# Performance work log

Measured on AMD Instinct MI355X. Metric: run time of the kernel, lower is better.

The kernel has to match this reference:

```python
import jax, jax.numpy as jnp
import numpy as np

B, S, E = 2, 1024, 1024
H, DH = 16, 64           # num_heads, key_dim = E // H
MAXLEN = 2048            # config.max_sequence_length -> table size 2*MAXLEN-1


def setup_inputs() -> dict:
    key = jax.random.key(0)
    ks = jax.random.split(key, 13)
    sc = 1.0 / np.sqrt(E)
    return {
        "query": jax.random.normal(ks[0], (B, S, E), jnp.float32),
        "key": jax.random.normal(ks[1], (B, S, E), jnp.float32),
        "value": jax.random.normal(ks[2], (B, S, E), jnp.float32),
        "Wq": jax.random.normal(ks[3], (E, E), jnp.float32) * sc,
        "bq": jnp.zeros((E,), jnp.float32),
        "Wk": jax.random.normal(ks[4], (E, E), jnp.float32) * sc,
        "bk": jnp.zeros((E,), jnp.float32),
        "Wv": jax.random.normal(ks[5], (E, E), jnp.float32) * sc,
        "bv": jnp.zeros((E,), jnp.float32),
        "Wo": jax.random.normal(ks[6], (E, E), jnp.float32) * sc,
        "bo": jnp.zeros((E,), jnp.float32),
        "rel_pos_emb": jax.random.normal(ks[7], (2 * MAXLEN - 1, DH), jnp.float32) * 0.02,
        "rel_pos_bias": jnp.zeros((2 * MAXLEN - 1,), jnp.float32),
    }


def _split_heads(x):
    # [B, S, E] -> [B, H, S, DH]
    return x.reshape(B, S, H, DH).transpose(0, 2, 1, 3)


def _relative_shift(x):
    # x: [B, H, S, S]; pad one zero column on the left of the last dim,
    # reshape to [B, H, S+1, S], drop the first row -> [B, H, S, S]
    x = jnp.pad(x, ((0, 0), (0, 0), (0, 0), (1, 0)))
    x = x.reshape(B, H, S + 1, S)
    return x[:, :, 1:, :]


def reference(query, key, value, Wq, bq, Wk, bk, Wv, bv, Wo, bo,
              rel_pos_emb, rel_pos_bias):
    q = _split_heads(query @ Wq + bq) / jnp.sqrt(jnp.float32(DH))  # [B,H,S,DH]
    k = _split_heads(key @ Wk + bk)                                 # [B,H,S,DH]
    v = _split_heads(value @ Wv + bv)                               # [B,H,S,DH]

    scores = jnp.einsum("bhid,bhjd->bhij", q, k)  # [B,H,S,S]

    # relative position term (gather + skew, as in the original call())
    pos_ids = jnp.arange(S)[:, None] - jnp.arange(S)[None, :] + (MAXLEN - 1)  # [S,S]
    rpe = rel_pos_emb[pos_ids]    # [S, S, DH]
    rpb = rel_pos_bias[pos_ids]   # [S, S]
    rel = jnp.einsum("bhid,ijd->bhij", q, rpe)  # [B,H,S,S]
    rel = _relative_shift(rel)
    scores = scores + rel + rpb   # rpb broadcasts over [B,H]

    weights = jax.nn.softmax(scores, axis=-1)
    out = jnp.einsum("bhij,bhjd->bhid", weights, v)  # [B,H,S,DH]
    out = out.transpose(0, 2, 1, 3).reshape(B, S, E)
    return out @ Wo + bo
```

## Files before the change

kernel.cpp:

```cpp
#include <hip/hip_runtime.h>

typedef unsigned short u16;
typedef __bf16 bf16_t;
typedef bf16_t bf16x8 __attribute__((ext_vector_type(8)));
typedef u16 u16x8 __attribute__((ext_vector_type(8)));
typedef float f32x4 __attribute__((ext_vector_type(4)));

#define DEVI __device__ __forceinline__


DEVI u16 f2bf(float f) {
    unsigned u = __builtin_bit_cast(unsigned, f);
    u = (u + 0x7FFFu + ((u >> 16) & 1u)) >> 16;
    return (u16)u;
}
DEVI float bf2f(u16 b) {
    unsigned u = ((unsigned)b) << 16;
    return __builtin_bit_cast(float, u);
}
DEVI f32x4 mfma16(u16x8 a, u16x8 b, f32x4 c) {
    return __builtin_amdgcn_mfma_f32_16x16x32_bf16(
        __builtin_bit_cast(bf16x8, a), __builtin_bit_cast(bf16x8, b), c, 0, 0, 0);
}
DEVI void gl2lds(const u16* g, u16* l) {
    __builtin_amdgcn_global_load_lds(
        (__attribute__((address_space(1))) void*)g,
        (__attribute__((address_space(3))) void*)l, 16, 0, 0);
}

__global__ __launch_bounds__(256) void cvt_kernel(
    const float* __restrict__ q, const float* __restrict__ k, const float* __restrict__ v,
    const float* __restrict__ emb, const float* __restrict__ rpb,
    u16* __restrict__ xq, u16* __restrict__ xk, u16* __restrict__ xv, u16* __restrict__ embb,
    u16* __restrict__ Brel2)
{
    const long NQ = 2097152;
    const long NE = 262080;
    if (blockIdx.x >= 6400) {
        int u = (blockIdx.x - 6400) * 256 + threadIdx.x;
        int i = u & 1023;
        if (i <= 1022)
            Brel2[((long)u << 10) + i + 1] = f2bf(rpb[2046]);
        return;
    }
    long i4 = ((long)blockIdx.x * 256 + threadIdx.x) * 4;
    if (i4 < 3 * NQ) {
        int which = (int)(i4 >> 21);
        long off = i4 & (NQ - 1);
        const float* src = which == 0 ? q : (which == 1 ? k : v);
        u16* dst = which == 0 ? xq : (which == 1 ? xk : xv);
        float4 f = *(const float4*)(src + off);
        ushort4 o; o.x = f2bf(f.x); o.y = f2bf(f.y); o.z = f2bf(f.z); o.w = f2bf(f.w);
        *(ushort4*)(dst + off) = o;
    } else {
        long off = i4 - 3 * NQ;
        if (off < NE) {
            float4 f = *(const float4*)(emb + off);
            ushort4 o; o.x = f2bf(f.x); o.y = f2bf(f.y); o.z = f2bf(f.z); o.w = f2bf(f.w);
            *(ushort4*)(embb + off) = o;
        }
    }
}

__global__ __launch_bounds__(256) void wt_kernel(
    const float* __restrict__ w0, const float* __restrict__ w1,
    const float* __restrict__ w2, const float* __restrict__ w3,
    u16* __restrict__ t0, u16* __restrict__ t1, u16* __restrict__ t2, u16* __restrict__ t3)
{
    int z = blockIdx.z;
    const float* W = z == 0 ? w0 : (z == 1 ? w1 : (z == 2 ? w2 : w3));
    u16* T = z == 0 ? t0 : (z == 1 ? t1 : (z == 2 ? t2 : t3));
    __shared__ float tile[64][65];
    int k0 = blockIdx.y * 64, n0 = blockIdx.x * 64;
    int tx = threadIdx.x, ty = threadIdx.y;
    for (int r = ty; r < 64; r += 4)
        tile[r][tx] = W[(long)(k0 + r) * 1024 + n0 + tx];
    __syncthreads();
    for (int r = ty; r < 64; r += 4)
        T[(long)(n0 + r) * 1024 + k0 + tx] = f2bf(tile[tx][r]);
}

template<int MT>
__global__ __launch_bounds__(256) void gemm_kernel(
    const u16* __restrict__ A0, const u16* __restrict__ A1, const u16* __restrict__ A2,
    const u16* __restrict__ W0, const u16* __restrict__ W1, const u16* __restrict__ W2,
    const float* __restrict__ bias0, const float* __restrict__ bias1, const float* __restrict__ bias2,
    u16* __restrict__ o0, u16* __restrict__ o1, u16* __restrict__ o2,
    float* __restrict__ ofp, int mode_base)
{
    int z = blockIdx.z;
    int mode = mode_base + z;
    const u16* A = z == 0 ? A0 : (z == 1 ? A1 : A2);
    const u16* W = z == 0 ? W0 : (z == 1 ? W1 : W2);
    const float* bias = z == 0 ? bias0 : (z == 1 ? bias1 : bias2);
    u16* ob = z == 0 ? o0 : (z == 1 ? o1 : o2);

    constexpr int MROWS = MT * 32;
    __shared__ u16 la[MROWS * 32];
    __shared__ u16 lw[128 * 32];

    int m0 = blockIdx.y * MROWS, n0 = blockIdx.x * 128;
    int t = threadIdx.x, lane = t & 63, wid = t >> 6;
    int l15 = lane & 15, quad = lane >> 4;
    int wm = (wid >> 1) * (MT * 16), wn = (wid & 1) * 64;
    int sr = lane >> 2, sp = lane & 3;

    f32x4 acc[MT][4] = {};

    for (int k0 = 0; k0 < 1024; k0 += 32) {
        __syncthreads();
#pragma unroll
        for (int q = 0; q < MT / 2; q++) {
            int r = wid * (MT * 8) + q * 16 + sr;
            int c = sp ^ ((r >> 1) & 3);
            gl2lds(A + (long)(m0 + r) * 1024 + k0 + c * 8, la + (wid * (MT * 8) + q * 16) * 32);
        }
#pragma unroll
        for (int q = 0; q < 2; q++) {
            int r = wid * 32 + q * 16 + sr;
            int c = sp ^ ((r >> 1) & 3);
            gl2lds(W + (long)(n0 + r) * 1024 + k0 + c * 8, lw + (wid * 32 + q * 16) * 32);
        }
        __syncthreads();
        u16x8 af[MT], bfr[4];
#pragma unroll
        for (int mt = 0; mt < MT; mt++) {
            int r = wm + mt * 16 + l15;
            af[mt] = *(const u16x8*)&la[r * 32 + ((quad ^ ((r >> 1) & 3)) * 8)];
        }
#pragma unroll
        for (int nt = 0; nt < 4; nt++) {
            int r = wn + nt * 16 + l15;
            bfr[nt] = *(const u16x8*)&lw[r * 32 + ((quad ^ ((r >> 1) & 3)) * 8)];
        }
#pragma unroll
        for (int mt = 0; mt < MT; mt++)
#pragma unroll
            for (int nt = 0; nt < 4; nt++)
                acc[mt][nt] = mfma16(af[mt], bfr[nt], acc[mt][nt]);
    }

#pragma unroll
    for (int mt = 0; mt < MT; mt++)
#pragma unroll
        for (int nt = 0; nt < 4; nt++)
#pragma unroll
            for (int reg = 0; reg < 4; reg++) {
                int gm = m0 + wm + mt * 16 + quad * 4 + reg;
                int gn = n0 + wn + nt * 16 + l15;
                float val = acc[mt][nt][reg] + bias[gn];
                if (mode == 0) {
                    val *= 0.125f;
                    long o = ((long)((gm >> 10) * 16 + (gn >> 6)) << 16) + ((gm & 1023) << 6) + (gn & 63);
                    ob[o] = f2bf(val);
                } else if (mode == 1) {
                    long o = ((long)((gm >> 10) * 16 + (gn >> 6)) << 16) + ((gm & 1023) << 6) + (gn & 63);
                    ob[o] = f2bf(val);
                } else if (mode == 2) {
                    long o = ((long)((gm >> 10) * 16 + (gn >> 6)) << 16) + ((long)(gn & 63) << 10) + (gm & 1023);
                    ob[o] = f2bf(val);
                } else {
                    ofp[(long)gm * 1024 + gn] = val;
                }
            }
}

__global__ __launch_bounds__(256) void gc_kernel(
    const u16* __restrict__ qb, const u16* __restrict__ embb,
    const float* __restrict__ rpb, u16* __restrict__ Brel2)
{
    int u0 = blockIdx.x * 16;
    int i0 = u0 & 1023;
    int t = threadIdx.x, lane = t & 63, wid = t >> 6;
    int l15 = lane & 15, quad = lane >> 4;

    u16x8 aq[2];
    long qoff = (long)(u0 + l15) * 64 + quad * 8;
    aq[0] = *(const u16x8*)&qb[qoff];
    aq[1] = *(const u16x8*)&qb[qoff + 32];

    for (int tt = wid; tt < 65; tt += 4) {
        int w0 = tt * 16;
        long ebase = (long)(1024 + i0 + w0 + l15) * 64 + quad * 8;
        u16x8 b0 = *(const u16x8*)&embb[ebase];
        u16x8 b1 = *(const u16x8*)&embb[ebase + 32];
        f32x4 c = {};
        c = mfma16(aq[0], b0, c);
        c = mfma16(aq[1], b1, c);
#pragma unroll
        for (int reg = 0; reg < 4; reg++) {
            int r = quad * 4 + reg;
            int cc = w0 + l15 - r;
            if (cc < 0 || cc > 1023) continue;
            int u = u0 + r;
            int i = u & 1023;
            if (cc <= i) {
                Brel2[((long)u << 10) + (i - cc)] = f2bf(c[reg] + rpb[cc + 2047]);
            } else if (i >= 1) {
                Brel2[((long)(u - 1) << 10) + (i + 1024 - cc)] = f2bf(c[reg] + rpb[cc + 1022]);
            }
        }
    }
}

__global__ __launch_bounds__(256, 4) void flash_kernel(
    const u16* __restrict__ qb, const u16* __restrict__ kb, const u16* __restrict__ vT,
    const u16* __restrict__ Brel2,
    float* __restrict__ Po, float* __restrict__ Pm, float* __restrict__ Pl)
{
    int itile = blockIdx.x;
    int bh = blockIdx.y;
    int js = blockIdx.z;
    int t = threadIdx.x, lane = t & 63, wid = t >> 6;
    int l15 = lane & 15, quad = lane >> 4;
    int i0w = itile * 64 + wid * 16;

    __shared__ u16 lds_k[64 * 64];
    __shared__ u16 lds_v[64 * 64];
    __shared__ u16 lds_p[4][16][72];

    int sr8 = lane >> 3, sp8 = lane & 7;

    u16x8 aq[2];
    {
        long qoff = ((long)(bh * 1024) + i0w + l15) * 64 + quad * 8;
        aq[0] = *(const u16x8*)&qb[qoff];
        aq[1] = *(const u16x8*)&qb[qoff + 32];
    }
    float m_r[4], l_r[4];
    f32x4 o_acc[4] = {};
#pragma unroll
    for (int r = 0; r < 4; r++) { m_r[r] = -1e30f; l_r[r] = 0.f; }

    const u16* kbase = kb + (long)bh * 65536;
    const u16* vbase = vT + (long)bh * 65536;
    const u16* bbase = Brel2 + ((long)bh << 20);

    for (int jt = 0; jt < 8; jt++) {
        int j0 = js * 512 + jt * 64;
        __syncthreads();
#pragma unroll
        for (int q = 0; q < 2; q++) {
            int r = wid * 16 + q * 8 + sr8;
            int c = sp8 ^ (r & 7);
            gl2lds(kbase + (long)(j0 + r) * 64 + c * 8, lds_k + (wid * 16 + q * 8) * 64);
            gl2lds(vbase + (long)r * 1024 + j0 + c * 8, lds_v + (wid * 16 + q * 8) * 64);
        }
        __syncthreads();

        f32x4 s_acc[4];
#pragma unroll
        for (int nt = 0; nt < 4; nt++) {
            int r = nt * 16 + l15;
            u16x8 b0 = *(const u16x8*)&lds_k[r * 64 + ((quad ^ (r & 7)) * 8)];
            u16x8 b1 = *(const u16x8*)&lds_k[r * 64 + (((quad + 4) ^ (r & 7)) * 8)];
            f32x4 c = {};
            c = mfma16(aq[0], b0, c);
            c = mfma16(aq[1], b1, c);
            s_acc[nt] = c;
        }

#pragma unroll
        for (int nt = 0; nt < 4; nt++) {
            int jj = j0 + nt * 16 + l15;
#pragma unroll
            for (int reg = 0; reg < 4; reg++) {
                int ii = i0w + quad * 4 + reg;
                s_acc[nt][reg] += bf2f(bbase[((long)ii << 10) + jj]);
            }
        }

#pragma unroll
        for (int reg = 0; reg < 4; reg++) {
            float mx = fmaxf(fmaxf(s_acc[0][reg], s_acc[1][reg]), fmaxf(s_acc[2][reg], s_acc[3][reg]));
            for (int off = 1; off < 16; off <<= 1) mx = fmaxf(mx, __shfl_xor(mx, off, 64));
            float mnew = fmaxf(m_r[reg], mx);
            float alpha = __expf(m_r[reg] - mnew);
            float rs = 0.f;
#pragma unroll
            for (int nt = 0; nt < 4; nt++) {
                float p = __expf(s_acc[nt][reg] - mnew);
                s_acc[nt][reg] = p;
                rs += p;
            }
            for (int off = 1; off < 16; off <<= 1) rs += __shfl_xor(rs, off, 64);
            l_r[reg] = l_r[reg] * alpha + rs;
            m_r[reg] = mnew;
#pragma unroll
            for (int dt = 0; dt < 4; dt++) o_acc[dt][reg] *= alpha;
        }

#pragma unroll
        for (int nt = 0; nt < 4; nt++)
#pragma unroll
            for (int reg = 0; reg < 4; reg++)
                lds_p[wid][quad * 4 + reg][nt * 16 + l15] = f2bf(s_acc[nt][reg]);

        u16x8 pf0 = *(const u16x8*)&lds_p[wid][l15][quad * 8];
        u16x8 pf1 = *(const u16x8*)&lds_p[wid][l15][quad * 8 + 32];
#pragma unroll
        for (int dt = 0; dt < 4; dt++) {
            int r = dt * 16 + l15;
            u16x8 v0 = *(const u16x8*)&lds_v[r * 64 + ((quad ^ (r & 7)) * 8)];
            u16x8 v1 = *(const u16x8*)&lds_v[r * 64 + (((quad + 4) ^ (r & 7)) * 8)];
            o_acc[dt] = mfma16(pf0, v0, o_acc[dt]);
            o_acc[dt] = mfma16(pf1, v1, o_acc[dt]);
        }
    }

    int blk = (js * 32 + bh) * 16 + itile;
    float* PoB = Po + (long)blk * 4096;
#pragma unroll
    for (int dt = 0; dt < 4; dt++)
#pragma unroll
        for (int reg = 0; reg < 4; reg++) {
            int rr = wid * 16 + quad * 4 + reg;
            PoB[rr * 64 + dt * 16 + l15] = o_acc[dt][reg];
        }
    if (l15 == 0) {
#pragma unroll
        for (int reg = 0; reg < 4; reg++) {
            int rr = wid * 16 + quad * 4 + reg;
            Pm[blk * 64 + rr] = m_r[reg];
            Pl[blk * 64 + rr] = l_r[reg];
        }
    }
}

__global__ __launch_bounds__(256) void combine_kernel(
    const float* __restrict__ Po, const float* __restrict__ Pm, const float* __restrict__ Pl,
    u16* __restrict__ attn)
{
    int itile = blockIdx.x, bh = blockIdx.y;
    int t = threadIdx.x;
    int c = t & 63, rg = t >> 6;
    int blk0 = bh * 16 + itile;
    int blk1 = (32 + bh) * 16 + itile;
    int b = bh >> 4, h = bh & 15;
    for (int rr = rg; rr < 64; rr += 4) {
        float m0 = Pm[blk0 * 64 + rr], m1 = Pm[blk1 * 64 + rr];
        float ms = fmaxf(m0, m1);
        float e0 = __expf(m0 - ms), e1 = __expf(m1 - ms);
        float l = Pl[blk0 * 64 + rr] * e0 + Pl[blk1 * 64 + rr] * e1;
        float o = Po[(long)blk0 * 4096 + rr * 64 + c] * e0
                + Po[(long)blk1 * 4096 + rr * 64 + c] * e1;
        int ii = itile * 64 + rr;
        attn[((long)(b * 1024 + ii)) * 1024 + h * 64 + c] = f2bf(o / l);
    }
}

extern "C" void kernel_launch(void* const* d_in, const int* in_sizes, int n_in,
                              void* d_out, int out_size, void* d_ws, size_t ws_size,
                              hipStream_t stream)
{
    const float* query = (const float*)d_in[0];
    const float* key_  = (const float*)d_in[1];
    const float* value = (const float*)d_in[2];
    const float* Wq = (const float*)d_in[3];
    const float* bq = (const float*)d_in[4];
    const float* Wk = (const float*)d_in[5];
    const float* bk = (const float*)d_in[6];
    const float* Wv = (const float*)d_in[7];
    const float* bv = (const float*)d_in[8];
    const float* Wo = (const float*)d_in[9];
    const float* bo = (const float*)d_in[10];
    const float* emb = (const float*)d_in[11];
    const float* rpb = (const float*)d_in[12];

    char* ws = (char*)d_ws;
    u16* xq   = (u16*)(ws + 0);
    u16* xk   = (u16*)(ws + 4194304);
    u16* xv   = (u16*)(ws + 8388608);
    u16* WqT  = (u16*)(ws + 12582912);
    u16* WkT  = (u16*)(ws + 14680064);
    u16* WvT  = (u16*)(ws + 16777216);
    u16* embb = (u16*)(ws + 18874368);
    u16* WoT  = (u16*)(ws + 19922944);
    u16* qb   = (u16*)(ws + 22020096);
    u16* kb   = (u16*)(ws + 26214400);
    u16* vT   = (u16*)(ws + 30408704);
    u16* Brel2= (u16*)(ws + 34603008);
    float* Po = (float*)(ws + 0);
    float* Pm = (float*)(ws + 16777216);
    float* Pl = (float*)(ws + 17039360);
    u16* attn = (u16*)(ws + 22020096);

    cvt_kernel<<<6528, 256, 0, stream>>>(query, key_, value, emb, rpb, xq, xk, xv, embb, Brel2);
    wt_kernel<<<dim3(16, 16, 4), dim3(64, 4), 0, stream>>>(Wq, Wk, Wv, Wo, WqT, WkT, WvT, WoT);
    gemm_kernel<4><<<dim3(8, 16, 3), 256, 0, stream>>>(xq, xk, xv, WqT, WkT, WvT,
                                                       bq, bk, bv, qb, kb, vT, nullptr, 0);
    gc_kernel<<<2048, 256, 0, stream>>>(qb, embb, rpb, Brel2);
    flash_kernel<<<dim3(16, 32, 2), 256, 0, stream>>>(qb, kb, vT, Brel2, Po, Pm, Pl);
    combine_kernel<<<dim3(16, 32), 256, 0, stream>>>(Po, Pm, Pl, attn);
    gemm_kernel<2><<<dim3(8, 32, 1), 256, 0, stream>>>(attn, nullptr, nullptr, WoT, nullptr, nullptr,
                                                       bo, nullptr, nullptr,
                                                       nullptr, nullptr, nullptr, (float*)d_out, 3);
}
```

Baseline: 250.7 us.

## Stage skewed relative-position scores in LDS for coalesced vectorized stores

The gc kernel now writes its MFMA results into a shared-memory tile laid out in the skewed order. It then has each thread write 8-element vectors to Brel2, adding the position bias during that pass. The boundary fill that cvt_kernel used to do is folded into this pass, so cvt_kernel no longer takes rpb or Brel2 and launches fewer blocks. The aim is to replace scattered 2-byte global stores with coalesced 16-byte stores. The cost is about 33KB of LDS per block, an extra barrier, and a second bf16 rounding before the bias is added.

```diff
diff --git a/kernel.cpp b/kernel.cpp
--- a/kernel.cpp
+++ b/kernel.cpp
@@ -30,19 +30,11 @@
 
 __global__ __launch_bounds__(256) void cvt_kernel(
     const float* __restrict__ q, const float* __restrict__ k, const float* __restrict__ v,
-    const float* __restrict__ emb, const float* __restrict__ rpb,
-    u16* __restrict__ xq, u16* __restrict__ xk, u16* __restrict__ xv, u16* __restrict__ embb,
-    u16* __restrict__ Brel2)
+    const float* __restrict__ emb,
+    u16* __restrict__ xq, u16* __restrict__ xk, u16* __restrict__ xv, u16* __restrict__ embb)
 {
     const long NQ = 2097152;
     const long NE = 262080;
-    if (blockIdx.x >= 6400) {
-        int u = (blockIdx.x - 6400) * 256 + threadIdx.x;
-        int i = u & 1023;
-        if (i <= 1022)
-            Brel2[((long)u << 10) + i + 1] = f2bf(rpb[2046]);
-        return;
-    }
     long i4 = ((long)blockIdx.x * 256 + threadIdx.x) * 4;
     if (i4 < 3 * NQ) {
         int which = (int)(i4 >> 21);
@@ -165,10 +157,12 @@
             }
 }
 
-__global__ __launch_bounds__(256) void gc_kernel(
+__global__ __launch_bounds__(256, 4) void gc_kernel(
     const u16* __restrict__ qb, const u16* __restrict__ embb,
     const float* __restrict__ rpb, u16* __restrict__ Brel2)
 {
+    __shared__ u16 Ls[16 * 1032];
+
     int u0 = blockIdx.x * 16;
     int i0 = u0 & 1023;
     int t = threadIdx.x, lane = t & 63, wid = t >> 6;
@@ -190,14 +184,57 @@
 #pragma unroll
         for (int reg = 0; reg < 4; reg++) {
             int r = quad * 4 + reg;
-            int cc = w0 + l15 - r;
+            int w = w0 + l15;
+            int cc = w - r;
             if (cc < 0 || cc > 1023) continue;
-            int u = u0 + r;
-            int i = u & 1023;
-            if (cc <= i) {
-                Brel2[((long)u << 10) + (i - cc)] = f2bf(c[reg] + rpb[cc + 2047]);
-            } else if (i >= 1) {
-                Brel2[((long)(u - 1) << 10) + (i + 1024 - cc)] = f2bf(c[reg] + rpb[cc + 1022]);
+            int jj = i0 + 2 * r - w;
+            if (jj < 0) jj += 1024;
+            Ls[r * 1032 + jj] = f2bf(c[reg]);
+        }
+    }
+    __syncthreads();
+
+    int r = t >> 4, p = t & 15;
+    int i = i0 + r, u = u0 + r;
+    const u16* lrow = Ls + r * 1032;
+
+    int hi1 = min(i + 1, 1023);
+    u16* out1 = Brel2 + ((long)u << 10);
+    for (int j0 = p * 8; j0 <= hi1; j0 += 128) {
+        if (j0 + 7 <= i) {
+            u16x8 g = *(const u16x8*)&lrow[j0];
+            u16x8 o;
+#pragma unroll
+            for (int e = 0; e < 8; e++)
+                o[e] = f2bf(bf2f(g[e]) + rpb[i - (j0 + e) + 2047]);
+            *(u16x8*)&out1[j0] = o;
+        } else {
+            for (int e = 0; e < 8; e++) {
+                int j = j0 + e;
+                if (j > hi1) break;
+                float v = (j == i + 1) ? 0.f : bf2f(lrow[j]);
+                out1[j] = f2bf(v + rpb[i - j + 2047]);
+            }
+        }
+    }
+
+    if (i != 0) {
+        int lo = i + 1;
+        u16* out2 = Brel2 + ((long)(u - 1) << 10);
+        for (int j0 = (lo & ~7) + p * 8; j0 <= 1023; j0 += 128) {
+            if (j0 >= lo) {
+                u16x8 g = *(const u16x8*)&lrow[j0];
+                u16x8 o;
+#pragma unroll
+                for (int e = 0; e < 8; e++)
+                    o[e] = f2bf(bf2f(g[e]) + rpb[i - (j0 + e) + 2046]);
+                *(u16x8*)&out2[j0] = o;
+            } else {
+                for (int e = 0; e < 8; e++) {
+                    int j = j0 + e;
+                    if (j >= lo)
+                        out2[j] = f2bf(bf2f(lrow[j]) + rpb[i - j + 2046]);
+                }
             }
         }
     }
@@ -385,7 +422,7 @@
     float* Pl = (float*)(ws + 17039360);
     u16* attn = (u16*)(ws + 22020096);
 
-    cvt_kernel<<<6528, 256, 0, stream>>>(query, key_, value, emb, rpb, xq, xk, xv, embb, Brel2);
+    cvt_kernel<<<6400, 256, 0, stream>>>(query, key_, value, emb, xq, xk, xv, embb);
     wt_kernel<<<dim3(16, 16, 4), dim3(64, 4), 0, stream>>>(Wq, Wk, Wv, Wo, WqT, WkT, WvT, WoT);
     gemm_kernel<4><<<dim3(8, 16, 3), 256, 0, stream>>>(xq, xk, xv, WqT, WkT, WvT,
                                                        bq, bk, bv, qb, kb, vT, nullptr, 0);
```

New measurement: 296.4 us. 1.18x slower.

## Store unskewed relative-position band and apply skew and bias inside flash kernel

Applied to the files above, without the earlier changes.

The gc kernel now writes a compact per-row band of q·emb products (row stride 1040) with contiguous vectorized stores, instead of scattering skewed bf16 values into a full S×S Brel2 matrix. The relative-shift indexing and the rpb bias lookup move into the flash kernel's score-add loop, and the cvt kernel no longer prefills the Brel2 constant region. The aim is to drop the scattered writes and the extra fill pass. In exchange the flash inner loop does more index arithmetic, a select and an extra rpb gather per element, and its bias reads are less coalesced.

```diff
diff --git a/kernel.cpp b/kernel.cpp
--- a/kernel.cpp
+++ b/kernel.cpp
@@ -4,6 +4,7 @@
 typedef __bf16 bf16_t;
 typedef bf16_t bf16x8 __attribute__((ext_vector_type(8)));
 typedef u16 u16x8 __attribute__((ext_vector_type(8)));
+typedef u16 u16x4 __attribute__((ext_vector_type(4)));
 typedef float f32x4 __attribute__((ext_vector_type(4)));
 
 #define DEVI __device__ __forceinline__
@@ -30,19 +31,11 @@
 
 __global__ __launch_bounds__(256) void cvt_kernel(
     const float* __restrict__ q, const float* __restrict__ k, const float* __restrict__ v,
-    const float* __restrict__ emb, const float* __restrict__ rpb,
-    u16* __restrict__ xq, u16* __restrict__ xk, u16* __restrict__ xv, u16* __restrict__ embb,
-    u16* __restrict__ Brel2)
+    const float* __restrict__ emb,
+    u16* __restrict__ xq, u16* __restrict__ xk, u16* __restrict__ xv, u16* __restrict__ embb)
 {
     const long NQ = 2097152;
     const long NE = 262080;
-    if (blockIdx.x >= 6400) {
-        int u = (blockIdx.x - 6400) * 256 + threadIdx.x;
-        int i = u & 1023;
-        if (i <= 1022)
-            Brel2[((long)u << 10) + i + 1] = f2bf(rpb[2046]);
-        return;
-    }
     long i4 = ((long)blockIdx.x * 256 + threadIdx.x) * 4;
     if (i4 < 3 * NQ) {
         int which = (int)(i4 >> 21);
@@ -165,47 +158,37 @@
             }
 }
 
-__global__ __launch_bounds__(256) void gc_kernel(
-    const u16* __restrict__ qb, const u16* __restrict__ embb,
-    const float* __restrict__ rpb, u16* __restrict__ Brel2)
+__global__ __launch_bounds__(256, 8) void gc_kernel(
+    const u16* __restrict__ qb, const u16* __restrict__ embb, u16* __restrict__ Gw)
 {
     int u0 = blockIdx.x * 16;
     int i0 = u0 & 1023;
     int t = threadIdx.x, lane = t & 63, wid = t >> 6;
     int l15 = lane & 15, quad = lane >> 4;
 
-    u16x8 aq[2];
     long qoff = (long)(u0 + l15) * 64 + quad * 8;
-    aq[0] = *(const u16x8*)&qb[qoff];
-    aq[1] = *(const u16x8*)&qb[qoff + 32];
+    u16x8 bq0 = *(const u16x8*)&qb[qoff];
+    u16x8 bq1 = *(const u16x8*)&qb[qoff + 32];
+
+    u16* orow = Gw + (long)(u0 + l15) * 1040 + quad * 4;
+    const u16* ebase0 = embb + (long)(1024 + i0 + l15) * 64 + quad * 8;
 
     for (int tt = wid; tt < 65; tt += 4) {
-        int w0 = tt * 16;
-        long ebase = (long)(1024 + i0 + w0 + l15) * 64 + quad * 8;
-        u16x8 b0 = *(const u16x8*)&embb[ebase];
-        u16x8 b1 = *(const u16x8*)&embb[ebase + 32];
+        const u16* ep = ebase0 + (long)tt * 1024;
+        u16x8 a0 = *(const u16x8*)ep;
+        u16x8 a1 = *(const u16x8*)(ep + 32);
         f32x4 c = {};
-        c = mfma16(aq[0], b0, c);
-        c = mfma16(aq[1], b1, c);
-#pragma unroll
-        for (int reg = 0; reg < 4; reg++) {
-            int r = quad * 4 + reg;
-            int cc = w0 + l15 - r;
-            if (cc < 0 || cc > 1023) continue;
-            int u = u0 + r;
-            int i = u & 1023;
-            if (cc <= i) {
-                Brel2[((long)u << 10) + (i - cc)] = f2bf(c[reg] + rpb[cc + 2047]);
-            } else if (i >= 1) {
-                Brel2[((long)(u - 1) << 10) + (i + 1024 - cc)] = f2bf(c[reg] + rpb[cc + 1022]);
-            }
-        }
+        c = mfma16(a0, bq0, c);
+        c = mfma16(a1, bq1, c);
+        u16x4 o;
+        o[0] = f2bf(c[0]); o[1] = f2bf(c[1]); o[2] = f2bf(c[2]); o[3] = f2bf(c[3]);
+        *(u16x4*)(orow + tt * 16) = o;
     }
 }
 
 __global__ __launch_bounds__(256, 4) void flash_kernel(
     const u16* __restrict__ qb, const u16* __restrict__ kb, const u16* __restrict__ vT,
-    const u16* __restrict__ Brel2,
+    const u16* __restrict__ Gw, const float* __restrict__ rpb,
     float* __restrict__ Po, float* __restrict__ Pm, float* __restrict__ Pl)
 {
     int itile = blockIdx.x;
@@ -234,7 +217,7 @@
 
     const u16* kbase = kb + (long)bh * 65536;
     const u16* vbase = vT + (long)bh * 65536;
-    const u16* bbase = Brel2 + ((long)bh << 20);
+    const u16* gwb = Gw + (long)bh * 1024 * 1040;
 
     for (int jt = 0; jt < 8; jt++) {
         int j0 = js * 512 + jt * 64;
@@ -265,8 +248,14 @@
             int jj = j0 + nt * 16 + l15;
 #pragma unroll
             for (int reg = 0; reg < 4; reg++) {
-                int ii = i0w + quad * 4 + reg;
-                s_acc[nt][reg] += bf2f(bbase[((long)ii << 10) + jj]);
+                int q4r = quad * 4 + reg;
+                int ii = i0w + q4r;
+                int c = ii - jj;
+                long a1 = (long)ii * 1040 + c + q4r;
+                long a2 = (long)(ii + 1) * 1040 + c + 1025 + ((q4r + 1) & 15);
+                long ga = (c >= 0) ? a1 : a2;
+                float gval = (c == -1) ? 0.f : bf2f(gwb[ga]);
+                s_acc[nt][reg] += gval + rpb[c + 2047];
             }
         }
 
@@ -375,22 +364,22 @@
     u16* WkT  = (u16*)(ws + 14680064);
     u16* WvT  = (u16*)(ws + 16777216);
     u16* embb = (u16*)(ws + 18874368);
-    u16* WoT  = (u16*)(ws + 19922944);
-    u16* qb   = (u16*)(ws + 22020096);
-    u16* kb   = (u16*)(ws + 26214400);
-    u16* vT   = (u16*)(ws + 30408704);
-    u16* Brel2= (u16*)(ws + 34603008);
+    u16* WoT  = (u16*)(ws + 19398656);
+    u16* qb   = (u16*)(ws + 21495808);
+    u16* kb   = (u16*)(ws + 25690112);
+    u16* vT   = (u16*)(ws + 29884416);
+    u16* Gw   = (u16*)(ws + 34078720);
     float* Po = (float*)(ws + 0);
     float* Pm = (float*)(ws + 16777216);
     float* Pl = (float*)(ws + 17039360);
-    u16* attn = (u16*)(ws + 22020096);
-
-    cvt_kernel<<<6528, 256, 0, stream>>>(query, key_, value, emb, rpb, xq, xk, xv, embb, Brel2);
+    u16* attn = (u16*)(ws + 21495808);
+
+    cvt_kernel<<<6400, 256, 0, stream>>>(query, key_, value, emb, xq, xk, xv, embb);
     wt_kernel<<<dim3(16, 16, 4), dim3(64, 4), 0, stream>>>(Wq, Wk, Wv, Wo, WqT, WkT, WvT, WoT);
     gemm_kernel<4><<<dim3(8, 16, 3), 256, 0, stream>>>(xq, xk, xv, WqT, WkT, WvT,
                                                        bq, bk, bv, qb, kb, vT, nullptr, 0);
-    gc_kernel<<<2048, 256, 0, stream>>>(qb, embb, rpb, Brel2);
-    flash_kernel<<<dim3(16, 32, 2), 256, 0, stream>>>(qb, kb, vT, Brel2, Po, Pm, Pl);
+    gc_kernel<<<2048, 256, 0, stream>>>(qb, embb, Gw);
+    flash_kernel<<<dim3(16, 32, 2), 256, 0, stream>>>(qb, kb, vT, Gw, rpb, Po, Pm, Pl);
     combine_kernel<<<dim3(16, 32), 256, 0, stream>>>(Po, Pm, Pl, attn);
     gemm_kernel<2><<<dim3(8, 32, 1), 256, 0, stream>>>(attn, nullptr, nullptr, WoT, nullptr, nullptr,
                                                        bo, nullptr, nullptr,
```

Result: slower. 299.6 us (+19.5%).
